# Kernel optimization log

Measured on AMD Instinct MI355X. Metric: run time of the kernel, lower is better.

Reference implementation:

```python
import jax, jax.numpy as jnp
import numpy as np

B, S, D, H, HD = 4, 2048, 1024, 16, 64
MLP = 4 * D
ROPE_BASE = 10000.0
TARGET_SPARSITY = 0.2


def _rotate_half(t):
    return jnp.concatenate([-t[..., HD // 2:], t[..., :HD // 2]], axis=-1)


def setup_inputs() -> dict:
    key = jax.random.key(0)
    ks = jax.random.split(key, 10)
    s = 0.02
    return {
        "x": jax.random.normal(ks[0], (B, S, D), jnp.float32),
        "gate_w": jax.random.normal(ks[1], (D, 1), jnp.float32) * s,
        "gate_b": jnp.zeros((1,), jnp.float32),
        "wq": jax.random.normal(ks[2], (D, D), jnp.float32) * s,
        "wk": jax.random.normal(ks[3], (D, D), jnp.float32) * s,
        "wv": jax.random.normal(ks[4], (D, D), jnp.float32) * s,
        "wo": jax.random.normal(ks[5], (D, D), jnp.float32) * s,
        "conv_w": jax.random.normal(ks[6], (D, 3), jnp.float32) * s,  # depthwise k=3
        "conv_b": jnp.zeros((D,), jnp.float32),
        "mlp_w1": jax.random.normal(ks[7], (D, MLP), jnp.float32) * s,
        "mlp_b1": jnp.zeros((MLP,), jnp.float32),
        "mlp_w2": jax.random.normal(ks[8], (MLP, D), jnp.float32) * s,
        "mlp_b2": jnp.zeros((D,), jnp.float32),
    }


def reference(x, gate_w, gate_b, wq, wk, wv, wo, conv_w, conv_b,
              mlp_w1, mlp_b1, mlp_w2, mlp_b2):
    # --- Router (eval path: hard threshold, mask_ste == active mask) ---
    logits = x @ gate_w + gate_b                    # [B,S,1]
    probs = jax.nn.sigmoid(logits)
    aux_loss = (probs.mean() - TARGET_SPARSITY) ** 2
    mask = (probs > 0.5).astype(x.dtype)            # [B,S,1]

    # --- Reflexive stream: causal depthwise conv (left pad 2) + MLP ---
    xp = jnp.pad(x, ((0, 0), (2, 0), (0, 0)))       # [B,S+2,D]
    x_conv = (xp[:, 0:S] * conv_w[:, 0]
              + xp[:, 1:S + 1] * conv_w[:, 1]
              + xp[:, 2:S + 2] * conv_w[:, 2] + conv_b)
    shallow = jax.nn.relu(x_conv @ mlp_w1 + mlp_b1) @ mlp_w2 + mlp_b2

    # --- Contextual stream: RoPE causal attention, queries gated by router ---
    q = (x @ wq).reshape(B, S, H, HD)
    k = (x @ wk).reshape(B, S, H, HD)
    v = (x @ wv).reshape(B, S, H, HD)

    pos = jnp.arange(S)
    inv_freq = 1.0 / (ROPE_BASE ** (jnp.arange(0, HD, 2, dtype=jnp.float32) / HD))
    freqs = pos[:, None].astype(jnp.float32) * inv_freq[None, :]
    emb = jnp.concatenate([freqs, freqs], axis=-1)  # [S,HD]
    cos = jnp.cos(emb)[None, :, None, :]
    sin = jnp.sin(emb)[None, :, None, :]
    q = q * cos + _rotate_half(q) * sin
    k = k * cos + _rotate_half(k) * sin

    scale = 1.0 / np.sqrt(HD)
    scores = jnp.einsum('bqhd,bkhd->bhqk', q, k) * scale
    causal = pos[:, None] >= pos[None, :]           # [S,S]
    scores = jnp.where(causal[None, None], scores, jnp.finfo(scores.dtype).min)
    attn = jax.nn.softmax(scores, axis=-1)
    ctx = jnp.einsum('bhqk,bkhd->bqhd', attn, v).reshape(B, S, D)
    ctx = (ctx @ wo) * mask                         # scatter back: only active queries contribute

    out = x + shallow + ctx
    return out, aux_loss
```

## Files before the change

kernel.cpp:

```cpp
#include <hip/hip_runtime.h>
#include <hip/hip_bf16.h>

#define DDIM 1024
#define SLEN 2048
#define NTOK 8192
#define MLPD 4096

typedef float f32x4 __attribute__((ext_vector_type(4)));
typedef __bf16 bf16x8 __attribute__((ext_vector_type(8)));

__device__ __forceinline__ void async16(void* lds, const void* g) {
  __builtin_amdgcn_global_load_lds(
      (__attribute__((address_space(1))) void*)g,
      (__attribute__((address_space(3))) void*)lds, 16, 0, 0);
}

__global__ __launch_bounds__(256) void prep_kernel(
    const float* __restrict__ x, const float* __restrict__ gate_w,
    const float* __restrict__ gate_b, const float* __restrict__ conv_w,
    const float* __restrict__ conv_b, __bf16* __restrict__ xb,
    __bf16* __restrict__ xcb, float* __restrict__ maskp,
    float* __restrict__ probsp) {
  const int tok = blockIdx.x, t = threadIdx.x;
  const int s = tok & (SLEN - 1);
  const float* xr = x + (size_t)tok * DDIM;
  float4 v = ((const float4*)xr)[t];
  float4 g = ((const float4*)gate_w)[t];
  float part = v.x * g.x + v.y * g.y + v.z * g.z + v.w * g.w;
#pragma unroll
  for (int d = 32; d; d >>= 1) part += __shfl_down(part, d);
  __shared__ float ws4[4];
  const int lane = t & 63, w = t >> 6;
  if (lane == 0) ws4[w] = part;
  __syncthreads();
  if (t == 0) {
    float logit = ws4[0] + ws4[1] + ws4[2] + ws4[3] + gate_b[0];
    float prob = 1.f / (1.f + __expf(-logit));
    probsp[tok] = prob;
    maskp[tok] = prob > 0.5f ? 1.f : 0.f;
  }
  union { ushort4 u; __bf16 b[4]; } xo;
  xo.b[0] = (__bf16)v.x; xo.b[1] = (__bf16)v.y;
  xo.b[2] = (__bf16)v.z; xo.b[3] = (__bf16)v.w;
  ((ushort4*)(xb + (size_t)tok * DDIM))[t] = xo.u;
  float4 zero4 = {0.f, 0.f, 0.f, 0.f};
  float4 m1 = (s >= 1) ? ((const float4*)(xr - DDIM))[t] : zero4;
  float4 m2 = (s >= 2) ? ((const float4*)(xr - 2 * DDIM))[t] : zero4;
  int d0 = t * 4;
  float vv[4] = {v.x, v.y, v.z, v.w};
  float a1[4] = {m1.x, m1.y, m1.z, m1.w};
  float a2[4] = {m2.x, m2.y, m2.z, m2.w};
  union { ushort4 u; __bf16 b[4]; } co;
#pragma unroll
  for (int i = 0; i < 4; ++i) {
    float c0 = conv_w[(d0 + i) * 3 + 0];
    float c1 = conv_w[(d0 + i) * 3 + 1];
    float c2 = conv_w[(d0 + i) * 3 + 2];
    float r = a2[i] * c0 + a1[i] * c1 + vv[i] * c2 + conv_b[d0 + i];
    co.b[i] = (__bf16)r;
  }
  ((ushort4*)(xcb + (size_t)tok * DDIM))[t] = co.u;
}

__global__ __launch_bounds__(256) void tcast_kernel(const float* __restrict__ src,
                                                    __bf16* __restrict__ dst,
                                                    int K, int N) {
  __shared__ __bf16 tile[64][65];
  const int n0 = blockIdx.x * 64, k0 = blockIdx.y * 64;
  const int t = threadIdx.x;
  const int cr = (t & 15) * 4;
#pragma unroll
  for (int i = 0; i < 4; ++i) {
    int rr = (t >> 4) + i * 16;
    float4 v = *(const float4*)(src + (size_t)(k0 + rr) * N + n0 + cr);
    tile[rr][cr + 0] = (__bf16)v.x; tile[rr][cr + 1] = (__bf16)v.y;
    tile[rr][cr + 2] = (__bf16)v.z; tile[rr][cr + 3] = (__bf16)v.w;
  }
  __syncthreads();
#pragma unroll
  for (int i = 0; i < 2; ++i) {
    int c = t + i * 256;
    int nl = c >> 3, koff = (c & 7) * 8;
    union { uint4 u; __bf16 b[8]; } o;
#pragma unroll
    for (int j = 0; j < 8; ++j) o.b[j] = tile[koff + j][nl];
    *(uint4*)(dst + (size_t)(n0 + nl) * K + k0 + koff) = o.u;
  }
}

template <int EPI>
__global__ __launch_bounds__(256, 3) void gemm_bt(
    const __bf16* __restrict__ A, const __bf16* __restrict__ Bt,
    const float* __restrict__ bias, const float* __restrict__ xres,
    const float* __restrict__ maskp, __bf16* __restrict__ Cb,
    float* __restrict__ Cf, int M, int N, int K) {
  __shared__ char smem[32768];
  char* As = smem;
  char* Bs = smem + 16384;
  const int t = threadIdx.x, lane = t & 63, w = t >> 6;
  const int nwg = gridDim.x * gridDim.y;
  const int wgid = blockIdx.y * gridDim.x + blockIdx.x;
  const int swz = (wgid & 7) * (nwg >> 3) + (wgid >> 3);
  const int m0 = (swz / gridDim.x) * 128, n0 = (swz % gridDim.x) * 128;
  const int wm = (w >> 1) * 64, wn = (w & 1) * 64;
  f32x4 acc[4][4] = {};
  const int nk = K >> 6;
  for (int kt = 0; kt < nk; ++kt) {
    const int k0 = kt << 6;
#pragma unroll
    for (int rd = 0; rd < 4; ++rd) {
      int o = ((rd * 4 + w) << 10) + (lane << 4);
      int row = o >> 7;
      int us = ((o >> 4) & 7) ^ (row & 7);
      async16(As + o, A + (size_t)(m0 + row) * K + k0 + us * 8);
      async16(Bs + o, Bt + (size_t)(n0 + row) * K + k0 + us * 8);
    }
    __syncthreads();
#pragma unroll
    for (int ks = 0; ks < 2; ++ks) {
      bf16x8 af[4], bfr[4];
#pragma unroll
      for (int mt = 0; mt < 4; ++mt) {
        int row = wm + mt * 16 + (lane & 15);
        int u = (ks * 4 + (lane >> 4)) ^ (row & 7);
        af[mt] = *(const bf16x8*)(As + row * 128 + u * 16);
      }
#pragma unroll
      for (int nt = 0; nt < 4; ++nt) {
        int row = wn + nt * 16 + (lane & 15);
        int u = (ks * 4 + (lane >> 4)) ^ (row & 7);
        bfr[nt] = *(const bf16x8*)(Bs + row * 128 + u * 16);
      }
#pragma unroll
      for (int mt = 0; mt < 4; ++mt)
#pragma unroll
        for (int nt = 0; nt < 4; ++nt)
          acc[mt][nt] = __builtin_amdgcn_mfma_f32_16x16x32_bf16(
              af[mt], bfr[nt], acc[mt][nt], 0, 0, 0);
    }
    __syncthreads();
  }
#pragma unroll
  for (int mt = 0; mt < 4; ++mt)
#pragma unroll
    for (int nt = 0; nt < 4; ++nt)
#pragma unroll
      for (int r = 0; r < 4; ++r) {
        int row = m0 + wm + mt * 16 + ((lane >> 4) << 2) + r;
        int col = n0 + wn + nt * 16 + (lane & 15);
        float v = acc[mt][nt][r];
        size_t idx = (size_t)row * N + col;
        if constexpr (EPI == 0) {
          Cb[idx] = (__bf16)v;
        } else if constexpr (EPI == 1) {
          v += bias[col];
          Cb[idx] = (__bf16)fmaxf(v, 0.f);
        } else if constexpr (EPI == 2) {
          Cf[idx] = xres[idx] + v + bias[col];
        } else {
          Cf[idx] += maskp[row] * v;
        }
      }
}

__global__ __launch_bounds__(256) void rope_kernel(__bf16* __restrict__ qkv) {
  __shared__ float snv[32], csv[32];
  const int tok = blockIdx.x, t = threadIdx.x;
  const int s = tok & (SLEN - 1);
  if (t < 32) {
    float invf = __builtin_amdgcn_exp2f(-(float)t * (13.28771238f / 32.f));
    float fr = (float)s * invf;
    snv[t] = sinf(fr);
    csv[t] = cosf(fr);
  }
  __syncthreads();
#pragma unroll
  for (int pp = 0; pp < 2; ++pp) {
    int p = t + pp * 256;
    int h = p >> 5, i = p & 31;
    float sn = snv[i], cs = csv[i];
    __bf16* qp = qkv + (size_t)tok * 3072 + h * 64 + i;
    float xq = (float)qp[0], yq = (float)qp[32];
    qp[0] = (__bf16)(xq * cs - yq * sn);
    qp[32] = (__bf16)(yq * cs + xq * sn);
    __bf16* kp = qp + 1024;
    float xk = (float)kp[0], yk = (float)kp[32];
    kp[0] = (__bf16)(xk * cs - yk * sn);
    kp[32] = (__bf16)(yk * cs + xk * sn);
  }
}

__device__ __forceinline__ void scatterV(char* Vdst, int w, int lane,
                                         float4 va, float4 vb) {
  union { float4 f; __bf16 bv[8]; } u0, u1;
  u0.f = va; u1.f = vb;
#pragma unroll
  for (int j = 0; j < 8; ++j) {
    int d = w * 8 + j;
    int by = d * 128 + (((lane >> 3) ^ (d & 7)) << 4) + ((lane & 7) << 1);
    *(__bf16*)(Vdst + by) = u0.bv[j];
    int d2 = d + 32;
    int by2 = d2 * 128 + (((lane >> 3) ^ (d2 & 7)) << 4) + ((lane & 7) << 1);
    *(__bf16*)(Vdst + by2) = u1.bv[j];
  }
}

__global__ __launch_bounds__(256, 3) void attn_kernel(const __bf16* __restrict__ qkv,
                                                      __bf16* __restrict__ ctx) {
  __shared__ char sm[32768];
  const int t = threadIdx.x, lane = t & 63, w = t >> 6;
  const int c = lane & 15, g = lane >> 4, g4 = g * 4;
  const int bh = blockIdx.y, h = bh & 15, b = bh >> 4;
  const size_t tokbase = (size_t)b * SLEN;
  const __bf16* qg = qkv + tokbase * 3072 + h * 64;
  const __bf16* kg = qg + 1024;
  const __bf16* vg = qg + 2048;
  const float SCL = 0.125f * 1.44269504f;
  char* Ps = sm + (w << 12);
  char* Ks = sm + 16384;
  char* Vs = sm + 24576;

  for (int ph = 0; ph < 2; ++ph) {
    const int qt = ph == 0 ? (int)blockIdx.x : 15 - (int)blockIdx.x;
    const int q0 = qt * 128;
#pragma unroll
    for (int rd = 0; rd < 4; ++rd) {
      int o = ((rd * 4 + w) << 10) + (lane << 4);
      int row = o >> 7;
      int us = ((o >> 4) & 7) ^ (row & 7);
      async16(sm + o, qg + (size_t)(q0 + row) * 3072 + us * 8);
    }
    __syncthreads();
    bf16x8 qb[2][2];
#pragma unroll
    for (int mt = 0; mt < 2; ++mt)
#pragma unroll
      for (int ks = 0; ks < 2; ++ks) {
        int row = w * 32 + mt * 16 + c;
        int u = (ks * 4 + g) ^ (row & 7);
        qb[mt][ks] = *(const bf16x8*)(sm + row * 128 + u * 16);
      }

    float m_run[2] = {-1e30f, -1e30f}, l_run[2] = {0.f, 0.f};
    f32x4 o_acc[2][4] = {};
    const int nkt = (q0 + 128) >> 6;
    const int wrow0 = q0 + w * 32;

    for (int kt = 0; kt < nkt; ++kt) {
      const int k0 = kt << 6;
#pragma unroll
      for (int rd = 0; rd < 2; ++rd) {
        int o = ((rd * 4 + w) << 10) + (lane << 4);
        int row = o >> 7;
        int us = ((o >> 4) & 7) ^ (row & 7);
        async16(Ks + o, kg + (size_t)(k0 + row) * 3072 + us * 8);
      }
      {
        float4 va = *(const float4*)(vg + (size_t)(k0 + lane) * 3072 + w * 8);
        float4 vb2 = *(const float4*)(vg + (size_t)(k0 + lane) * 3072 + w * 8 + 32);
        scatterV(Vs, w, lane, va, vb2);
      }
      __syncthreads();
      if (k0 <= wrow0 + 31) {
        f32x4 st[4][2] = {};
        __builtin_amdgcn_s_setprio(1);
#pragma unroll
        for (int ks = 0; ks < 2; ++ks) {
          bf16x8 ka[4];
#pragma unroll
          for (int nt = 0; nt < 4; ++nt) {
            int row = nt * 16 + c;
            int u = (ks * 4 + g) ^ (row & 7);
            ka[nt] = *(const bf16x8*)(Ks + row * 128 + u * 16);
          }
#pragma unroll
          for (int nt = 0; nt < 4; ++nt)
#pragma unroll
            for (int mt = 0; mt < 2; ++mt)
              st[nt][mt] = __builtin_amdgcn_mfma_f32_16x16x32_bf16(
                  ka[nt], qb[mt][ks], st[nt][mt], 0, 0, 0);
        }
        __builtin_amdgcn_s_setprio(0);
        const bool needmask = (k0 + 63) > wrow0;
#pragma unroll
        for (int mt = 0; mt < 2; ++mt) {
          float mx = -1e30f;
          if (needmask) {
            int qglob = wrow0 + mt * 16 + c;
#pragma unroll
            for (int nt = 0; nt < 4; ++nt)
#pragma unroll
              for (int r = 0; r < 4; ++r) {
                float sv = st[nt][mt][r] * SCL;
                if (k0 + nt * 16 + g4 + r > qglob) sv = -1e30f;
                st[nt][mt][r] = sv;
                mx = fmaxf(mx, sv);
              }
          } else {
#pragma unroll
            for (int nt = 0; nt < 4; ++nt)
#pragma unroll
              for (int r = 0; r < 4; ++r) {
                float sv = st[nt][mt][r] * SCL;
                st[nt][mt][r] = sv;
                mx = fmaxf(mx, sv);
              }
          }
          mx = fmaxf(mx, __shfl_xor(mx, 16));
          mx = fmaxf(mx, __shfl_xor(mx, 32));
          const bool skip = __all(mx - m_run[mt] <= 8.f) != 0;
          float mnew = skip ? m_run[mt] : fmaxf(m_run[mt], mx);
          float rs = 0.f;
#pragma unroll
          for (int nt = 0; nt < 4; ++nt)
#pragma unroll
            for (int r = 0; r < 4; ++r) {
              float p = __builtin_amdgcn_exp2f(st[nt][mt][r] - mnew);
              st[nt][mt][r] = p;
              rs += p;
            }
          rs += __shfl_xor(rs, 16);
          rs += __shfl_xor(rs, 32);
          if (skip) {
            l_run[mt] += rs;
          } else {
            float fac = __builtin_amdgcn_exp2f(m_run[mt] - mnew);
            m_run[mt] = mnew;
            l_run[mt] = l_run[mt] * fac + rs;
#pragma unroll
            for (int r = 0; r < 4; ++r) {
              float fr = __shfl(fac, g * 20 + r);
#pragma unroll
              for (int dt = 0; dt < 4; ++dt) o_acc[mt][dt][r] *= fr;
            }
          }
          int rowq = mt * 16 + c;
          int rbase = rowq * 128 + 8 * (g & 1);
#pragma unroll
          for (int nt = 0; nt < 4; ++nt) {
            int us = (2 * nt + (g >> 1)) ^ (c & 7);
            union { uint2 v; __bf16 bb[4]; } pp;
            pp.bb[0] = (__bf16)st[nt][mt][0]; pp.bb[1] = (__bf16)st[nt][mt][1];
            pp.bb[2] = (__bf16)st[nt][mt][2]; pp.bb[3] = (__bf16)st[nt][mt][3];
            *(uint2*)(Ps + rbase + us * 16) = pp.v;
          }
        }
        __builtin_amdgcn_s_setprio(1);
#pragma unroll
        for (int ks = 0; ks < 2; ++ks) {
          bf16x8 pa[2], vb[4];
#pragma unroll
          for (int mt = 0; mt < 2; ++mt) {
            int row = mt * 16 + c;
            int u = (ks * 4 + g) ^ (row & 7);
            pa[mt] = *(const bf16x8*)(Ps + row * 128 + u * 16);
          }
#pragma unroll
          for (int dt = 0; dt < 4; ++dt) {
            int row = dt * 16 + c;
            int u = (ks * 4 + g) ^ (row & 7);
            vb[dt] = *(const bf16x8*)(Vs + row * 128 + u * 16);
          }
#pragma unroll
          for (int mt = 0; mt < 2; ++mt)
#pragma unroll
            for (int dt = 0; dt < 4; ++dt)
              o_acc[mt][dt] = __builtin_amdgcn_mfma_f32_16x16x32_bf16(
                  pa[mt], vb[dt], o_acc[mt][dt], 0, 0, 0);
        }
        __builtin_amdgcn_s_setprio(0);
      }
      __syncthreads();
    }
#pragma unroll
    for (int mt = 0; mt < 2; ++mt)
#pragma unroll
      for (int r = 0; r < 4; ++r) {
        float lr = __shfl(l_run[mt], g * 20 + r);
        float inv = 1.f / lr;
        int tokr = q0 + w * 32 + mt * 16 + g4 + r;
#pragma unroll
        for (int dt = 0; dt < 4; ++dt) {
          int d = dt * 16 + c;
          ctx[(tokbase + tokr) * DDIM + h * 64 + d] =
              (__bf16)(o_acc[mt][dt][r] * inv);
        }
      }
  }
}

__global__ __launch_bounds__(256) void aux_kernel(const float* __restrict__ probsp,
                                                  float* __restrict__ outp) {
  const int t = threadIdx.x;
  float sum = 0.f;
  for (int i = t; i < NTOK; i += 256) sum += probsp[i];
#pragma unroll
  for (int d = 32; d; d >>= 1) sum += __shfl_down(sum, d);
  __shared__ float ws4[4];
  if ((t & 63) == 0) ws4[t >> 6] = sum;
  __syncthreads();
  if (t == 0) {
    float m = (ws4[0] + ws4[1] + ws4[2] + ws4[3]) * (1.f / NTOK) - 0.2f;
    outp[0] = m * m;
  }
}

extern "C" void kernel_launch(void* const* d_in, const int* in_sizes, int n_in,
                              void* d_out, int out_size, void* d_ws, size_t ws_size,
                              hipStream_t stream) {
  const float* x      = (const float*)d_in[0];
  const float* gate_w = (const float*)d_in[1];
  const float* gate_b = (const float*)d_in[2];
  const float* wq     = (const float*)d_in[3];
  const float* wk     = (const float*)d_in[4];
  const float* wv     = (const float*)d_in[5];
  const float* wo     = (const float*)d_in[6];
  const float* conv_w = (const float*)d_in[7];
  const float* conv_b = (const float*)d_in[8];
  const float* mlp_w1 = (const float*)d_in[9];
  const float* mlp_b1 = (const float*)d_in[10];
  const float* mlp_w2 = (const float*)d_in[11];
  const float* mlp_b2 = (const float*)d_in[12];
  float* out = (float*)d_out;

  char* ws = (char*)d_ws;
  const size_t MB = 1ull << 20;
  __bf16* xb     = (__bf16*)(ws + 0);
  __bf16* xcb    = (__bf16*)(ws + 16 * MB);
  __bf16* ctx    = (__bf16*)(ws + 16 * MB);
  __bf16* wqkv_t = (__bf16*)(ws + 32 * MB);
  __bf16* wo_t   = (__bf16*)(ws + 38 * MB);
  __bf16* w1_t   = (__bf16*)(ws + 40 * MB);
  __bf16* w2_t   = (__bf16*)(ws + 48 * MB);
  float*  maskp  = (float*)(ws + 56 * MB);
  float*  probsp = (float*)(ws + 56 * MB + 65536);
  __bf16* h1     = (__bf16*)(ws + 57 * MB);
  __bf16* qkv    = (__bf16*)(ws + 57 * MB);

  prep_kernel<<<NTOK, 256, 0, stream>>>(x, gate_w, gate_b, conv_w, conv_b,
                                        xb, xcb, maskp, probsp);
  tcast_kernel<<<dim3(16, 16), 256, 0, stream>>>(wq, wqkv_t, 1024, 1024);
  tcast_kernel<<<dim3(16, 16), 256, 0, stream>>>(wk, wqkv_t + 1024 * 1024, 1024, 1024);
  tcast_kernel<<<dim3(16, 16), 256, 0, stream>>>(wv, wqkv_t + 2048 * 1024, 1024, 1024);
  tcast_kernel<<<dim3(16, 16), 256, 0, stream>>>(wo, wo_t, 1024, 1024);
  tcast_kernel<<<dim3(64, 16), 256, 0, stream>>>(mlp_w1, w1_t, 1024, 4096);
  tcast_kernel<<<dim3(16, 64), 256, 0, stream>>>(mlp_w2, w2_t, 4096, 1024);

  gemm_bt<1><<<dim3(32, 64), 256, 0, stream>>>(xcb, w1_t, mlp_b1, nullptr, nullptr,
                                               h1, nullptr, NTOK, MLPD, DDIM);
  gemm_bt<2><<<dim3(8, 64), 256, 0, stream>>>(h1, w2_t, mlp_b2, x, nullptr,
                                              nullptr, out, NTOK, DDIM, MLPD);
  gemm_bt<0><<<dim3(24, 64), 256, 0, stream>>>(xb, wqkv_t, nullptr, nullptr, nullptr,
                                               qkv, nullptr, NTOK, 3072, DDIM);
  rope_kernel<<<NTOK, 256, 0, stream>>>(qkv);
  attn_kernel<<<dim3(8, 64), 256, 0, stream>>>(qkv, ctx);
  gemm_bt<3><<<dim3(8, 64), 256, 0, stream>>>(ctx, wo_t, nullptr, nullptr, maskp,
                                              nullptr, out, NTOK, DDIM, DDIM);
  aux_kernel<<<1, 256, 0, stream>>>(probsp, out + (size_t)(out_size - 1));
}
```

Measured before the change: 402.3 us.

## Add 256x256 double-buffered GEMM for MLP-up and QKV projections

Adds a new 512-thread GEMM kernel with 256x256 output tiles, a double-buffered 128KB LDS layout with XOR swizzling, and async global-to-LDS prefetch interleaved with MFMA compute, using setprio around the MFMA blocks. The MLP up-projection (ReLU epilogue) and the fused QKV projection now use it in place of the 128x128 single-buffered kernel. The aim is more data reuse per LDS byte and overlap of loads with compute. The cost is heavy register pressure (32 accumulators per wave) and large dynamic LDS, which may limit occupancy, plus fewer workgroups in the grid.

Measured after the change: 401.8 us. About the same (-0.1%).

```diff
diff --git a/kernel.cpp b/kernel.cpp
--- a/kernel.cpp
+++ b/kernel.cpp
@@ -86,6 +86,103 @@
     for (int j = 0; j < 8; ++j) o.b[j] = tile[koff + j][nl];
     *(uint4*)(dst + (size_t)(n0 + nl) * K + k0 + koff) = o.u;
   }
+}
+
+template <int EPI>
+__global__ __launch_bounds__(512, 2) void gemm256(
+    const __bf16* __restrict__ A, const __bf16* __restrict__ Bt,
+    const float* __restrict__ bias, __bf16* __restrict__ Cb,
+    int M, int N, int K) {
+  extern __shared__ char sm[];
+  const int t = threadIdx.x, lane = t & 63, w = t >> 6;
+  const int c = lane & 15, g = lane >> 4;
+  const int nwg = gridDim.x * gridDim.y;
+  const int wgid = blockIdx.y * gridDim.x + blockIdx.x;
+  const int swz = (wgid & 7) * (nwg >> 3) + (wgid >> 3);
+  const int m0 = (swz / gridDim.x) * 256, n0 = (swz % gridDim.x) * 256;
+  const int ha = w >> 2;
+  const int hb = (w & 3) >> 1;
+  const int bro = (w & 1) * 64;
+
+  f32x4 acc[8][4] = {};
+  const int nk = K >> 6;
+
+  auto stage = [&](int buf, int kind, int k0) {
+#pragma unroll
+    for (int r = 0; r < 2; ++r) {
+      int o = ((r * 8 + w) << 10) + (lane << 4);
+      int row = o >> 7;
+      int us = ((o >> 4) & 7) ^ (row & 7);
+      const __bf16* src =
+          (kind < 2) ? A + (size_t)(m0 + kind * 128 + row) * K + k0 + us * 8
+                     : Bt + (size_t)(n0 + (kind - 2) * 128 + row) * K + k0 + us * 8;
+      async16(sm + buf * 65536 + kind * 16384 + o, src);
+    }
+  };
+
+#pragma unroll
+  for (int kind = 0; kind < 4; ++kind) stage(0, kind, 0);
+  __syncthreads();
+
+  int cur = 0;
+  for (int kt = 0; kt < nk; ++kt) {
+    const int k0n = (kt + 1) << 6;
+    const bool pref = (kt + 1) < nk;
+    const char* Ab = sm + cur * 65536 + ha * 16384;
+    const char* Bb = sm + cur * 65536 + 32768 + hb * 16384;
+    bf16x8 bq[4];
+#pragma unroll
+    for (int ks = 0; ks < 2; ++ks) {
+#pragma unroll
+      for (int mh = 0; mh < 2; ++mh) {
+        const int p = ks * 2 + mh;
+        if (pref) stage(cur ^ 1, p, k0n);
+        if (mh == 0) {
+#pragma unroll
+          for (int nt = 0; nt < 4; ++nt) {
+            int row = bro + nt * 16 + c;
+            int u = (ks * 4 + g) ^ (row & 7);
+            bq[nt] = *(const bf16x8*)(Bb + row * 128 + u * 16);
+          }
+        }
+        bf16x8 aq[4];
+#pragma unroll
+        for (int i = 0; i < 4; ++i) {
+          int row = (mh * 4 + i) * 16 + c;
+          int u = (ks * 4 + g) ^ (row & 7);
+          aq[i] = *(const bf16x8*)(Ab + row * 128 + u * 16);
+        }
+        __builtin_amdgcn_s_setprio(1);
+#pragma unroll
+        for (int i = 0; i < 4; ++i)
+#pragma unroll
+          for (int nt = 0; nt < 4; ++nt)
+            acc[mh * 4 + i][nt] = __builtin_amdgcn_mfma_f32_16x16x32_bf16(
+                aq[i], bq[nt], acc[mh * 4 + i][nt], 0, 0, 0);
+        __builtin_amdgcn_s_setprio(0);
+      }
+    }
+    __syncthreads();
+    cur ^= 1;
+  }
+  const int wm = (w >> 2) * 128, wn = (w & 3) * 64;
+#pragma unroll
+  for (int mt = 0; mt < 8; ++mt)
+#pragma unroll
+    for (int nt = 0; nt < 4; ++nt)
+#pragma unroll
+      for (int r = 0; r < 4; ++r) {
+        int row = m0 + wm + mt * 16 + g * 4 + r;
+        int col = n0 + wn + nt * 16 + c;
+        float v = acc[mt][nt][r];
+        size_t idx = (size_t)row * N + col;
+        if constexpr (EPI == 0) {
+          Cb[idx] = (__bf16)v;
+        } else {
+          v += bias[col];
+          Cb[idx] = (__bf16)fmaxf(v, 0.f);
+        }
+      }
 }
 
 template <int EPI>
@@ -150,12 +247,7 @@
         int col = n0 + wn + nt * 16 + (lane & 15);
         float v = acc[mt][nt][r];
         size_t idx = (size_t)row * N + col;
-        if constexpr (EPI == 0) {
-          Cb[idx] = (__bf16)v;
-        } else if constexpr (EPI == 1) {
-          v += bias[col];
-          Cb[idx] = (__bf16)fmaxf(v, 0.f);
-        } else if constexpr (EPI == 2) {
+        if constexpr (EPI == 2) {
           Cf[idx] = xres[idx] + v + bias[col];
         } else {
           Cf[idx] += maskp[row] * v;
@@ -446,12 +538,12 @@
   tcast_kernel<<<dim3(64, 16), 256, 0, stream>>>(mlp_w1, w1_t, 1024, 4096);
   tcast_kernel<<<dim3(16, 64), 256, 0, stream>>>(mlp_w2, w2_t, 4096, 1024);
 
-  gemm_bt<1><<<dim3(32, 64), 256, 0, stream>>>(xcb, w1_t, mlp_b1, nullptr, nullptr,
-                                               h1, nullptr, NTOK, MLPD, DDIM);
+  gemm256<1><<<dim3(16, 32), 512, 131072, stream>>>(xcb, w1_t, mlp_b1, h1,
+                                                    NTOK, MLPD, DDIM);
   gemm_bt<2><<<dim3(8, 64), 256, 0, stream>>>(h1, w2_t, mlp_b2, x, nullptr,
                                               nullptr, out, NTOK, DDIM, MLPD);
-  gemm_bt<0><<<dim3(24, 64), 256, 0, stream>>>(xb, wqkv_t, nullptr, nullptr, nullptr,
-                                               qkv, nullptr, NTOK, 3072, DDIM);
+  gemm256<0><<<dim3(12, 32), 512, 131072, stream>>>(xb, wqkv_t, nullptr, qkv,
+                                                    NTOK, 3072, DDIM);
   rope_kernel<<<NTOK, 256, 0, stream>>>(qkv);
   attn_kernel<<<dim3(8, 64), 256, 0, stream>>>(qkv, ctx);
   gemm_bt<3><<<dim3(8, 64), 256, 0, stream>>>(ctx, wo_t, nullptr, nullptr, maskp,
```

## Add 256x256 four-stage pipelined GEMM for MLP up-projection and QKV

Applied to the files above, without the earlier changes.

Introduces a new GEMM kernel with 256x256 tiles, 512 threads and a 4-deep async global-to-LDS pipeline with XOR-swizzled LDS layout and explicit vmcnt waits. It is used for the MLP first layer and the QKV projection, replacing the 128x128 kernel. Larger tiles raise arithmetic intensity and the multi-stage prefetch hides load latency, at the cost of 128KB dynamic LDS per block, which limits occupancy, and fewer blocks, which can leave some CUs with uneven work.

After: 405.7 us. No clear change (+0.8%).

```diff
diff --git a/kernel.cpp b/kernel.cpp
--- a/kernel.cpp
+++ b/kernel.cpp
@@ -14,6 +14,8 @@
       (__attribute__((address_space(1))) void*)g,
       (__attribute__((address_space(3))) void*)lds, 16, 0, 0);
 }
+
+template <int N> struct VMC { static constexpr int v = N; };
 
 __global__ __launch_bounds__(256) void prep_kernel(
     const float* __restrict__ x, const float* __restrict__ gate_w,
@@ -86,6 +88,101 @@
     for (int j = 0; j < 8; ++j) o.b[j] = tile[koff + j][nl];
     *(uint4*)(dst + (size_t)(n0 + nl) * K + k0 + koff) = o.u;
   }
+}
+
+template <int EPI>
+__global__ __launch_bounds__(512, 2) void gemm256p(
+    const __bf16* __restrict__ A, const __bf16* __restrict__ Bt,
+    const float* __restrict__ bias, __bf16* __restrict__ Cb,
+    int M, int N, int K) {
+  extern __shared__ char sm[];
+  const int t = threadIdx.x, lane = t & 63, w = t >> 6;
+  const int c = lane & 15, g = lane >> 4;
+  const int nwg = gridDim.x * gridDim.y;
+  const int wgid = blockIdx.y * gridDim.x + blockIdx.x;
+  const int swz = (wgid & 7) * (nwg >> 3) + (wgid >> 3);
+  const int m0 = (swz / gridDim.x) * 256, n0 = (swz % gridDim.x) * 256;
+  const int wm = (w >> 2) * 128, wn = (w & 3) * 64;
+
+  f32x4 acc[8][4] = {};
+  const int nk = K >> 5;
+
+  auto stage = [&](int buf, int kt) {
+    const int k0 = kt << 5;
+    char* base = sm + buf * 32768;
+#pragma unroll
+    for (int r = 0; r < 2; ++r) {
+      int o = ((r * 8 + w) << 10) + (lane << 4);
+      int rp = o >> 7;
+      int u = (o >> 4) & 7;
+      int l = u ^ (rp & 7);
+      int mr = rp * 2 + (l >> 2);
+      int kk = (l & 3) * 8;
+      async16(base + o, A + (size_t)(m0 + mr) * K + k0 + kk);
+      async16(base + 16384 + o, Bt + (size_t)(n0 + mr) * K + k0 + kk);
+    }
+  };
+
+  auto body = [&](auto vmc, int tt, bool dostage) {
+    if (dostage) stage((tt + 3) & 3, tt + 3);
+    asm volatile("s_waitcnt vmcnt(%0)" ::"n"(decltype(vmc)::v) : "memory");
+    __builtin_amdgcn_s_barrier();
+    asm volatile("" ::: "memory");
+    const char* Ab = sm + (tt & 3) * 32768;
+    const char* Bb = Ab + 16384;
+    bf16x8 aq[8], bq[4];
+#pragma unroll
+    for (int nt = 0; nt < 4; ++nt) {
+      int row = wn + nt * 16 + c;
+      int rp = row >> 1;
+      int u = ((row & 1) * 4 + g) ^ (rp & 7);
+      bq[nt] = *(const bf16x8*)(Bb + rp * 128 + u * 16);
+    }
+#pragma unroll
+    for (int i = 0; i < 8; ++i) {
+      int row = wm + i * 16 + c;
+      int rp = row >> 1;
+      int u = ((row & 1) * 4 + g) ^ (rp & 7);
+      aq[i] = *(const bf16x8*)(Ab + rp * 128 + u * 16);
+    }
+    __builtin_amdgcn_s_setprio(1);
+#pragma unroll
+    for (int i = 0; i < 8; ++i)
+#pragma unroll
+      for (int nt = 0; nt < 4; ++nt)
+        acc[i][nt] = __builtin_amdgcn_mfma_f32_16x16x32_bf16(
+            aq[i], bq[nt], acc[i][nt], 0, 0, 0);
+    __builtin_amdgcn_s_setprio(0);
+    __builtin_amdgcn_s_barrier();
+    asm volatile("" ::: "memory");
+  };
+
+  stage(0, 0);
+  stage(1, 1);
+  stage(2, 2);
+  int tt = 0;
+  for (; tt < nk - 3; ++tt) body(VMC<12>{}, tt, true);
+  body(VMC<8>{}, tt, false); ++tt;
+  body(VMC<4>{}, tt, false); ++tt;
+  body(VMC<0>{}, tt, false);
+
+#pragma unroll
+  for (int i = 0; i < 8; ++i)
+#pragma unroll
+    for (int nt = 0; nt < 4; ++nt)
+#pragma unroll
+      for (int r = 0; r < 4; ++r) {
+        int row = m0 + wm + i * 16 + g * 4 + r;
+        int col = n0 + wn + nt * 16 + c;
+        float v = acc[i][nt][r];
+        size_t idx = (size_t)row * N + col;
+        if constexpr (EPI == 0) {
+          Cb[idx] = (__bf16)v;
+        } else {
+          v += bias[col];
+          Cb[idx] = (__bf16)fmaxf(v, 0.f);
+        }
+      }
 }
 
 template <int EPI>
@@ -150,12 +247,7 @@
         int col = n0 + wn + nt * 16 + (lane & 15);
         float v = acc[mt][nt][r];
         size_t idx = (size_t)row * N + col;
-        if constexpr (EPI == 0) {
-          Cb[idx] = (__bf16)v;
-        } else if constexpr (EPI == 1) {
-          v += bias[col];
-          Cb[idx] = (__bf16)fmaxf(v, 0.f);
-        } else if constexpr (EPI == 2) {
+        if constexpr (EPI == 2) {
           Cf[idx] = xres[idx] + v + bias[col];
         } else {
           Cf[idx] += maskp[row] * v;
@@ -446,12 +538,12 @@
   tcast_kernel<<<dim3(64, 16), 256, 0, stream>>>(mlp_w1, w1_t, 1024, 4096);
   tcast_kernel<<<dim3(16, 64), 256, 0, stream>>>(mlp_w2, w2_t, 4096, 1024);
 
-  gemm_bt<1><<<dim3(32, 64), 256, 0, stream>>>(xcb, w1_t, mlp_b1, nullptr, nullptr,
-                                               h1, nullptr, NTOK, MLPD, DDIM);
+  gemm256p<1><<<dim3(16, 32), 512, 131072, stream>>>(xcb, w1_t, mlp_b1, h1,
+                                                     NTOK, MLPD, DDIM);
   gemm_bt<2><<<dim3(8, 64), 256, 0, stream>>>(h1, w2_t, mlp_b2, x, nullptr,
                                               nullptr, out, NTOK, DDIM, MLPD);
-  gemm_bt<0><<<dim3(24, 64), 256, 0, stream>>>(xb, wqkv_t, nullptr, nullptr, nullptr,
-                                               qkv, nullptr, NTOK, 3072, DDIM);
+  gemm256p<0><<<dim3(12, 32), 512, 131072, stream>>>(xb, wqkv_t, nullptr, qkv,
+                                                     NTOK, 3072, DDIM);
   rope_kernel<<<NTOK, 256, 0, stream>>>(qkv);
   attn_kernel<<<dim3(8, 64), 256, 0, stream>>>(qkv, ctx);
   gemm_bt<3><<<dim3(8, 64), 256, 0, stream>>>(ctx, wo_t, nullptr, nullptr, maskp,
```
